# Kernel optimization log

Hardware: AMD Instinct MI355X
Metric: run time of the kernel (lower is better)

The kernel has to match this reference:

```python
import jax, jax.numpy as jnp
import numpy as np

EPS = 1e-8
HIDDEN = 200


def _dsmall(n, d):
    # torch: d = d*(d>eps) + eps*(d<=eps); n/d
    return n / jnp.where(d > EPS, d, EPS)


def _mp_match(v1, v2, w):
    # v1: (B,S,H); v2: (B,S,H) or (B,H); w: (L,H) -> (B,S,L)
    wt = w.T[None, None]                      # (1,1,H,L)
    a = v1[..., None] * wt                    # (B,S,H,L)
    if v2.ndim == 2:
        v2 = jnp.broadcast_to(v2[:, None, :], v1.shape)
    b = v2[..., None] * wt                    # (B,S,H,L)
    dot = jnp.sum(a * b, axis=2)
    na = jnp.linalg.norm(a, axis=2)
    nb = jnp.linalg.norm(b, axis=2)
    return dot / jnp.maximum(na * nb, EPS)    # cosine_similarity over H


def _mp_pairwise(v1, v2, w):
    # v1: (B,S1,H); v2: (B,S2,H); w: (L,H) -> (B,S1,S2,L)
    a = v1[:, None] * w[None, :, None]        # (B,L,S1,H)
    b = v2[:, None] * w[None, :, None]        # (B,L,S2,H)
    na = jnp.linalg.norm(a, axis=3, keepdims=True)   # (B,L,S1,1)
    nb = jnp.linalg.norm(b, axis=3, keepdims=True)   # (B,L,S2,1)
    n = jnp.einsum('blph,blqh->blpq', a, b)
    d = na * jnp.swapaxes(nb, 2, 3)
    return jnp.transpose(_dsmall(n, d), (0, 2, 3, 1))


def _attention(v1, v2):
    # cosine-similarity matrix (B,S1,S2)
    n1 = jnp.linalg.norm(v1, axis=2, keepdims=True)           # (B,S1,1)
    n2 = jnp.linalg.norm(v2, axis=2, keepdims=True)           # (B,S2,1)
    a = jnp.einsum('bph,bqh->bpq', v1, v2)
    return _dsmall(a, n1 * jnp.swapaxes(n2, 1, 2))


def _matching(con_p, con_h, w1, w2, w3, w4, w5, w6, w7, w8):
    p_fw, p_bw = con_p[..., :HIDDEN], con_p[..., HIDDEN:]
    h_fw, h_bw = con_h[..., :HIDDEN], con_h[..., HIDDEN:]

    # 1) full matching
    mv_p_full_fw = _mp_match(p_fw, h_fw[:, -1, :], w1)
    mv_p_full_bw = _mp_match(p_bw, h_bw[:, 0, :], w2)
    mv_h_full_fw = _mp_match(h_fw, p_fw[:, -1, :], w1)
    mv_h_full_bw = _mp_match(h_bw, p_bw[:, 0, :], w2)

    # 2) maxpooling matching
    mv_max_fw = _mp_pairwise(p_fw, h_fw, w3)  # (B,S1,S2,L)
    mv_max_bw = _mp_pairwise(p_bw, h_bw, w4)
    mv_p_max_fw = jnp.max(mv_max_fw, axis=2)
    mv_p_max_bw = jnp.max(mv_max_bw, axis=2)
    mv_h_max_fw = jnp.max(mv_max_fw, axis=1)
    mv_h_max_bw = jnp.max(mv_max_bw, axis=1)

    # 3) attentive matching (mean)
    att_fw = _attention(p_fw, h_fw)           # (B,S1,S2)
    att_bw = _attention(p_bw, h_bw)

    # sum of att_h over dim 2 is a matmul (same math, no (B,S1,S2,H) tensor)
    att_h_sum_fw = jnp.einsum('bpq,bqh->bph', att_fw, h_fw)
    att_h_sum_bw = jnp.einsum('bpq,bqh->bph', att_bw, h_bw)
    att_p_sum_fw = jnp.einsum('bpq,bph->bqh', att_fw, p_fw)
    att_p_sum_bw = jnp.einsum('bpq,bph->bqh', att_bw, p_bw)

    att_mean_h_fw = _dsmall(att_h_sum_fw, jnp.sum(att_fw, axis=2, keepdims=True))
    att_mean_h_bw = _dsmall(att_h_sum_bw, jnp.sum(att_bw, axis=2, keepdims=True))
    att_mean_p_fw = _dsmall(att_p_sum_fw, jnp.swapaxes(jnp.sum(att_fw, axis=1, keepdims=True), 1, 2))
    att_mean_p_bw = _dsmall(att_p_sum_bw, jnp.swapaxes(jnp.sum(att_bw, axis=1, keepdims=True), 1, 2))

    mv_p_att_mean_fw = _mp_match(p_fw, att_mean_h_fw, w5)
    mv_p_att_mean_bw = _mp_match(p_bw, att_mean_h_bw, w6)
    mv_h_att_mean_fw = _mp_match(h_fw, att_mean_p_fw, w5)
    mv_h_att_mean_bw = _mp_match(h_bw, att_mean_p_bw, w6)

    # 4) max-attentive matching (needs full (B,S1,S2,H) broadcast for the max)
    att_h_fw = h_fw[:, None, :, :] * att_fw[:, :, :, None]   # (B,S1,S2,H)
    att_h_bw = h_bw[:, None, :, :] * att_bw[:, :, :, None]
    att_p_fw = p_fw[:, :, None, :] * att_fw[:, :, :, None]
    att_p_bw = p_bw[:, :, None, :] * att_bw[:, :, :, None]

    att_max_h_fw = jnp.max(att_h_fw, axis=2)                 # (B,S1,H)
    att_max_h_bw = jnp.max(att_h_bw, axis=2)
    att_max_p_fw = jnp.max(att_p_fw, axis=1)                 # (B,S2,H)
    att_max_p_bw = jnp.max(att_p_bw, axis=1)

    mv_p_att_max_fw = _mp_match(p_fw, att_max_h_fw, w7)
    mv_p_att_max_bw = _mp_match(p_bw, att_max_h_bw, w8)
    mv_h_att_max_fw = _mp_match(h_fw, att_max_p_fw, w7)
    mv_h_att_max_bw = _mp_match(h_bw, att_max_p_bw, w8)

    mv_p = jnp.concatenate([mv_p_full_fw, mv_p_max_fw, mv_p_att_mean_fw, mv_p_att_max_fw,
                            mv_p_full_bw, mv_p_max_bw, mv_p_att_mean_bw, mv_p_att_max_bw], axis=2)
    mv_h = jnp.concatenate([mv_h_full_fw, mv_h_max_fw, mv_h_att_mean_fw, mv_h_att_max_fw,
                            mv_h_full_bw, mv_h_max_bw, mv_h_att_mean_bw, mv_h_att_max_bw], axis=2)
    # dropout is identity in inference mode
    return mv_p, mv_h


def setup_inputs() -> dict:
    key = jax.random.key(0)
    ks = jax.random.split(key, 10)
    B, S, H, L = 32, 64, HIDDEN, 20
    w_std = np.sqrt(2.0 / H)  # kaiming_normal fan_in
    inp = {
        'con_p': jax.random.normal(ks[0], (B, S, 2 * H), dtype=jnp.float32),
        'con_h': jax.random.normal(ks[1], (B, S, 2 * H), dtype=jnp.float32),
    }
    for i in range(8):
        inp[f'mp_w{i+1}'] = jax.random.normal(ks[2 + i], (L, H), dtype=jnp.float32) * w_std
    return inp


def reference(con_p, con_h, mp_w1, mp_w2, mp_w3, mp_w4, mp_w5, mp_w6, mp_w7, mp_w8):
    return _matching(con_p, con_h, mp_w1, mp_w2, mp_w3, mp_w4, mp_w5, mp_w6, mp_w7, mp_w8)
```

## Files before the change

### kernel.cpp

```cpp
#include <hip/hip_runtime.h>
#include <hip/hip_bf16.h>
#include <math.h>

#define EPS 1e-8f
#define BB 32
#define SS 64
#define HH 200
#define LL 20
#define KST 232
#define SST 68
#define MHS 200

typedef short bf16x8 __attribute__((ext_vector_type(8)));
typedef float f32x4 __attribute__((ext_vector_type(4)));

__device__ inline float bf2f(short u) {
    union { unsigned int i; float f; } v;
    v.i = ((unsigned int)(unsigned short)u) << 16;
    return v.f;
}

__global__ __launch_bounds__(512) void fused_all_kernel(
        const float* __restrict__ conp, const float* __restrict__ conh,
        const float* __restrict__ w1, const float* __restrict__ w2,
        const float* __restrict__ w3, const float* __restrict__ w4,
        const float* __restrict__ w5, const float* __restrict__ w6,
        const float* __restrict__ w7, const float* __restrict__ w8,
        float* __restrict__ out) {
    __shared__ __align__(16) float smem[19392];
    int t = threadIdx.x;

    int wg = ((blockIdx.x & 7) * 224) + (blockIdx.x >> 3);
    int grp = wg / 7;
    int rem = wg % 7;

    if (rem < 2) {
        __hip_bfloat16* AT = (__hip_bfloat16*)smem;
        __hip_bfloat16* BT = (__hip_bfloat16*)(smem + 1856);
        float* S_L  = smem + 9280;
        float* nrmA = smem + 10368;
        float* nrmB = smem + 10384;
        __hip_bfloat16* PB = (__hip_bfloat16*)smem;
        __hip_bfloat16* WB = (__hip_bfloat16*)(smem + 9280);
        float* meanL = smem + 12992;
        float* maxL  = smem + 16192;

        int blk = grp * 2 + rem;
        int qh = blk & 3;
        int sdb = blk >> 2;
        int b = sdb & 31, sd = sdb >> 5;
        int dir = sd & 1, side = sd >> 1;
        const float* selfb = side ? conh : conp;
        const float* oppb  = side ? conp : conh;
        int fidx = dir ? 0 : (SS - 1);
        const float* fvr = oppb + (b * SS + fidx) * (2 * HH) + dir * HH;

        int arow = t / 25, ack = t % 25;

        float xr[8], yv0[8];
        if (t < 400) {
            const float* xp = selfb + (b * SS + qh * 16 + arow) * (2 * HH) + dir * HH + ack * 8;
            *(float4*)&xr[0] = *(const float4*)xp; *(float4*)&xr[4] = *(const float4*)(xp + 4);
            *(float4*)&yv0[0] = *(const float4*)(fvr + ack * 8);
            *(float4*)&yv0[4] = *(const float4*)(fvr + ack * 8 + 4);
            __align__(16) __hip_bfloat16 r8[8];
#pragma unroll
            for (int i = 0; i < 8; ++i) r8[i] = __float2bfloat16(xr[i]);
            *(bf16x8*)&AT[arow * KST + ack * 8] = *(bf16x8*)r8;
        }
        {
            __align__(16) __hip_bfloat16 z8[8];
#pragma unroll
            for (int i = 0; i < 8; ++i) z8[i] = __float2bfloat16(0.f);
            if (t < 240) {
                if (t < 48) { int row = t / 3, ckp = 25 + t % 3;
                    *(bf16x8*)&AT[row * KST + ckp * 8] = *(bf16x8*)z8;
                } else { int e2 = t - 48; int row = e2 / 3, ckp = 25 + e2 % 3;
                    *(bf16x8*)&BT[row * KST + ckp * 8] = *(bf16x8*)z8;
                }
            }
        }
        for (int e = t; e < 1600; e += 512) {
            int rw = e / 25, ck = e % 25, k = ck * 8;
            const float* xp = oppb + (b * SS + rw) * (2 * HH) + dir * HH + k;
            float xv[8];
            *(float4*)&xv[0] = *(const float4*)xp; *(float4*)&xv[4] = *(const float4*)(xp + 4);
            __align__(16) __hip_bfloat16 r8[8];
#pragma unroll
            for (int i = 0; i < 8; ++i) r8[i] = __float2bfloat16(xv[i]);
            *(bf16x8*)&BT[rw * KST + k] = *(bf16x8*)r8;
        }
        __syncthreads();

        int wv_ = __builtin_amdgcn_readfirstlane(t >> 6);
        int lane = t & 63;
        int q = lane >> 4, c = lane & 15;

        if (wv_ < 4) {
            int ct = wv_;
            f32x4 acc = (f32x4){0.f, 0.f, 0.f, 0.f};
            for (int ks = 0; ks < 7; ++ks) {
                int kb = ks * 32 + q * 8;
                bf16x8 af  = *(const bf16x8*)&AT[c * KST + kb];
                bf16x8 bf_ = *(const bf16x8*)&BT[(ct * 16 + c) * KST + kb];
                acc = __builtin_amdgcn_mfma_f32_16x16x32_bf16(af, bf_, acc, 0, 0, 0);
            }
            int col = ct * 16 + c;
#pragma unroll
            for (int r = 0; r < 4; ++r) S_L[(q * 4 + r) * SST + col] = acc[r];
        } else {
            int dt = wv_ - 4;
            f32x4 accB = (f32x4){0.f, 0.f, 0.f, 0.f};
            for (int ks = 0; ks < 7; ++ks) {
                int kb = ks * 32 + q * 8;
                bf16x8 bf_ = *(const bf16x8*)&BT[(dt * 16 + c) * KST + kb];
                accB = __builtin_amdgcn_mfma_f32_16x16x32_bf16(bf_, bf_, accB, 0, 0, 0);
            }
            if ((c >> 2) == q) nrmB[dt * 16 + c] = accB[c & 3];
            if (dt == 0) {
                f32x4 accA = (f32x4){0.f, 0.f, 0.f, 0.f};
                for (int ks = 0; ks < 7; ++ks) {
                    int kb = ks * 32 + q * 8;
                    bf16x8 af = *(const bf16x8*)&AT[c * KST + kb];
                    accA = __builtin_amdgcn_mfma_f32_16x16x32_bf16(af, af, accA, 0, 0, 0);
                }
                if ((c >> 2) == q) nrmA[c] = accA[c & 3];
            }
        }
        __syncthreads();

        for (int e = t; e < 1024; e += 512) {
            int r_ = e >> 6, cc = e & 63;
            float ns = sqrtf(nrmA[r_]), no = sqrtf(nrmB[cc]);
            S_L[r_ * SST + cc] = S_L[r_ * SST + cc] / fmaxf(ns * no, EPS);
        }
        __syncthreads();

        float wf0[8], wf1[8], wf2[8];
        if (t < 500) {
            int wl = t / 25, wck = t % 25;
            const float* wp0 = (dir ? w2 : w1) + wl * HH + wck * 8;
            const float* wp1 = (dir ? w6 : w5) + wl * HH + wck * 8;
            const float* wp2 = (dir ? w8 : w7) + wl * HH + wck * 8;
            *(float4*)&wf0[0] = *(const float4*)wp0; *(float4*)&wf0[4] = *(const float4*)(wp0 + 4);
            *(float4*)&wf1[0] = *(const float4*)wp1; *(float4*)&wf1[4] = *(const float4*)(wp1 + 4);
            *(float4*)&wf2[0] = *(const float4*)wp2; *(float4*)&wf2[4] = *(const float4*)(wp2 + 4);
        }

        if (t < 400) {
            int s = arow, h0 = ack * 8;
            float sm = 0.f;
            float ms[8], mx[8];
#pragma unroll
            for (int i = 0; i < 8; ++i) { ms[i] = 0.f; mx[i] = -INFINITY; }
            for (int k = 0; k < 64; ++k) {
                float a = S_L[s * SST + k];
                sm += a;
                bf16x8 ov = *(const bf16x8*)&BT[k * KST + h0];
#pragma unroll
                for (int i = 0; i < 8; ++i) {
                    float tt = a * bf2f(ov[i]);
                    ms[i] += tt;
                    mx[i] = fmaxf(mx[i], tt);
                }
            }
            float dsv = fmaxf(sm, EPS);
#pragma unroll
            for (int i = 0; i < 8; ++i) ms[i] /= dsv;
            *(float4*)&meanL[s * MHS + h0]     = *(float4*)&ms[0];
            *(float4*)&meanL[s * MHS + h0 + 4] = *(float4*)&ms[4];
            *(float4*)&maxL[s * MHS + h0]      = *(float4*)&mx[0];
            *(float4*)&maxL[s * MHS + h0 + 4]  = *(float4*)&mx[4];
        }
        __syncthreads();

#pragma unroll
        for (int m = 0; m < 3; ++m) {
            if (t < 400) {
                float yv[8];
                if (m == 0) {
#pragma unroll
                    for (int i = 0; i < 8; ++i) yv[i] = yv0[i];
                } else {
                    const float* yL = (m == 1 ? meanL : maxL) + arow * MHS + ack * 8;
                    *(float4*)&yv[0] = *(const float4*)yL;
                    *(float4*)&yv[4] = *(const float4*)(yL + 4);
                }
                __align__(16) __hip_bfloat16 r1[8], r2[8];
#pragma unroll
                for (int i = 0; i < 8; ++i) {
                    r1[i] = __float2bfloat16(xr[i] * yv[i]);
                    r2[i] = __float2bfloat16(yv[i] * yv[i]);
                }
                if (m == 0) {
                    __align__(16) __hip_bfloat16 r0[8];
#pragma unroll
                    for (int i = 0; i < 8; ++i) r0[i] = __float2bfloat16(xr[i] * xr[i]);
                    *(bf16x8*)&PB[(0 * 16 + arow) * KST + ack * 8] = *(bf16x8*)r0;
                }
                *(bf16x8*)&PB[(1 * 16 + arow) * KST + ack * 8] = *(bf16x8*)r1;
                *(bf16x8*)&PB[(2 * 16 + arow) * KST + ack * 8] = *(bf16x8*)r2;
            }
            if (t < 500) {
                int wl = t / 25, wck = t % 25;
                __align__(16) __hip_bfloat16 wr[8];
                if (m == 0) {
#pragma unroll
                    for (int i = 0; i < 8; ++i) wr[i] = __float2bfloat16(wf0[i] * wf0[i]);
                } else if (m == 1) {
#pragma unroll
                    for (int i = 0; i < 8; ++i) wr[i] = __float2bfloat16(wf1[i] * wf1[i]);
                } else {
#pragma unroll
                    for (int i = 0; i < 8; ++i) wr[i] = __float2bfloat16(wf2[i] * wf2[i]);
                }
                *(bf16x8*)&WB[wl * KST + wck * 8] = *(bf16x8*)wr;
            }
            if (m == 0) {
                __align__(16) __hip_bfloat16 z8[8];
#pragma unroll
                for (int i = 0; i < 8; ++i) z8[i] = __float2bfloat16(0.f);
                for (int e = t; e < 540; e += 512) {
                    if (e < 144) { int row = e / 3, ckp = 25 + e % 3;
                        *(bf16x8*)&PB[row * KST + ckp * 8] = *(bf16x8*)z8;
                    } else if (e < 480) { int e2 = e - 144; int row = 20 + e2 / 28, ckp = e2 % 28;
                        *(bf16x8*)&WB[row * KST + ckp * 8] = *(bf16x8*)z8;
                    } else { int e2 = e - 480; int row = e2 / 3, ckp = 25 + e2 % 3;
                        *(bf16x8*)&WB[row * KST + ckp * 8] = *(bf16x8*)z8;
                    }
                }
            }
            __syncthreads();

            if (wv_ < 2) {
                int ntile = wv_;
                f32x4 accA = (f32x4){0.f, 0.f, 0.f, 0.f};
                f32x4 accD = (f32x4){0.f, 0.f, 0.f, 0.f};
                f32x4 accB = (f32x4){0.f, 0.f, 0.f, 0.f};
                for (int ks = 0; ks < 7; ++ks) {
                    int kb = ks * 32 + q * 8;
                    bf16x8 bfw = *(const bf16x8*)&WB[(ntile * 16 + c) * KST + kb];
                    bf16x8 a0 = *(const bf16x8*)&PB[(0 * 16 + c) * KST + kb];
                    bf16x8 a1 = *(const bf16x8*)&PB[(1 * 16 + c) * KST + kb];
                    bf16x8 a2 = *(const bf16x8*)&PB[(2 * 16 + c) * KST + kb];
                    accA = __builtin_amdgcn_mfma_f32_16x16x32_bf16(a0, bfw, accA, 0, 0, 0);
                    accD = __builtin_amdgcn_mfma_f32_16x16x32_bf16(a1, bfw, accD, 0, 0, 0);
                    accB = __builtin_amdgcn_mfma_f32_16x16x32_bf16(a2, bfw, accB, 0, 0, 0);
                }
                int l_ = ntile * 16 + c;
                if (l_ < LL) {
                    int chunk = (m == 0) ? 0 : (m == 1) ? 40 : 60;
#pragma unroll
                    for (int r = 0; r < 4; ++r) {
                        int s = qh * 16 + q * 4 + r;
                        float cosv = accD[r] / fmaxf(sqrtf(accA[r] * accB[r]), EPS);
                        out[side * (BB * SS * 160) + (b * SS + s) * 160 + dir * 80 + chunk + l_] = cosv;
                    }
                }
            }
            if (m < 2) __syncthreads();
        }
    } else {
        __hip_bfloat16* AT = (__hip_bfloat16*)smem;
        __hip_bfloat16* BT = (__hip_bfloat16*)(smem + 7424);
        float* cmL = smem + 14848;
        float* nA  = smem + 15104;
        float* nB  = smem + 15168;
        int blk = grp * 5 + (rem - 2);
        int l = blk % LL; int db = blk / LL; int b = db & 31; int dir = db >> 5;

        const float* wrow = (dir ? w4 : w3) + l * HH;
        const float* Ag = conp + dir * HH;
        const float* Bg = conh + dir * HH;

        for (int e = t; e < 64 * 28; e += 512) {
            int m = e / 28, ck = e - m * 28;
            int k = ck * 8;
            __align__(16) __hip_bfloat16 at8[8];
            __align__(16) __hip_bfloat16 bt8[8];
            if (k < HH) {
                const float* ap = Ag + (b * SS + m) * (2 * HH) + k;
                const float* bp = Bg + (b * SS + m) * (2 * HH) + k;
                const float* wp = wrow + k;
                float av[8], bv[8], wvv[8];
                *(float4*)&av[0]  = *(const float4*)ap; *(float4*)&av[4]  = *(const float4*)(ap + 4);
                *(float4*)&bv[0]  = *(const float4*)bp; *(float4*)&bv[4]  = *(const float4*)(bp + 4);
                *(float4*)&wvv[0] = *(const float4*)wp; *(float4*)&wvv[4] = *(const float4*)(wp + 4);
#pragma unroll
                for (int i = 0; i < 8; ++i) {
                    at8[i] = __float2bfloat16(av[i] * wvv[i]);
                    bt8[i] = __float2bfloat16(bv[i] * wvv[i]);
                }
            } else {
#pragma unroll
                for (int ii = 0; ii < 8; ++ii) { at8[ii] = __float2bfloat16(0.f); bt8[ii] = __float2bfloat16(0.f); }
            }
            *(bf16x8*)&AT[m * KST + k] = *(bf16x8*)at8;
            *(bf16x8*)&BT[m * KST + k] = *(bf16x8*)bt8;
        }
        __syncthreads();

        int wv_ = __builtin_amdgcn_readfirstlane(t >> 6);
        int lane = t & 63;
        int q = lane >> 4, c = lane & 15;
        int m0 = wv_ * 16;

        f32x4 acc[4];
#pragma unroll
        for (int ct = 0; ct < 4; ++ct) acc[ct] = (f32x4){0.f, 0.f, 0.f, 0.f};

        if (wv_ < 4) {
            for (int ks = 0; ks < 7; ++ks) {
                int kb = ks * 32 + q * 8;
                bf16x8 af = *(const bf16x8*)&AT[(m0 + c) * KST + kb];
#pragma unroll
                for (int ct = 0; ct < 4; ++ct) {
                    bf16x8 bf_ = *(const bf16x8*)&BT[(ct * 16 + c) * KST + kb];
                    acc[ct] = __builtin_amdgcn_mfma_f32_16x16x32_bf16(af, bf_, acc[ct], 0, 0, 0);
                }
            }
        } else {
            int d0 = (wv_ - 4) * 16;
            f32x4 accA = (f32x4){0.f, 0.f, 0.f, 0.f};
            f32x4 accB = (f32x4){0.f, 0.f, 0.f, 0.f};
            for (int ks = 0; ks < 7; ++ks) {
                int kb = ks * 32 + q * 8;
                bf16x8 af = *(const bf16x8*)&AT[(d0 + c) * KST + kb];
                bf16x8 bf_ = *(const bf16x8*)&BT[(d0 + c) * KST + kb];
                accA = __builtin_amdgcn_mfma_f32_16x16x32_bf16(af, af, accA, 0, 0, 0);
                accB = __builtin_amdgcn_mfma_f32_16x16x32_bf16(bf_, bf_, accB, 0, 0, 0);
            }
            if ((c >> 2) == q) { nA[d0 + c] = accA[c & 3]; nB[d0 + c] = accB[c & 3]; }
        }
        __syncthreads();

        if (wv_ < 4) {
            float na[4], nb[4];
#pragma unroll
            for (int r = 0; r < 4; ++r) na[r] = sqrtf(nA[m0 + q * 4 + r]);
#pragma unroll
            for (int ct = 0; ct < 4; ++ct) nb[ct] = sqrtf(nB[ct * 16 + c]);

            float rowm[4] = {-INFINITY, -INFINITY, -INFINITY, -INFINITY};
            float colm[4] = {-INFINITY, -INFINITY, -INFINITY, -INFINITY};
#pragma unroll
            for (int ct = 0; ct < 4; ++ct) {
#pragma unroll
                for (int r = 0; r < 4; ++r) {
                    float cv = acc[ct][r] / fmaxf(na[r] * nb[ct], EPS);
                    rowm[r] = fmaxf(rowm[r], cv);
                    colm[ct] = fmaxf(colm[ct], cv);
                }
            }

#pragma unroll
            for (int r = 0; r < 4; ++r) {
                float v = rowm[r];
                v = fmaxf(v, __shfl_xor(v, 1, 64));
                v = fmaxf(v, __shfl_xor(v, 2, 64));
                v = fmaxf(v, __shfl_xor(v, 4, 64));
                v = fmaxf(v, __shfl_xor(v, 8, 64));
                rowm[r] = v;
            }
            if (c == 0) {
#pragma unroll
                for (int r = 0; r < 4; ++r) {
                    int i = m0 + q * 4 + r;
                    out[(b * SS + i) * 160 + dir * 80 + 20 + l] = rowm[r];
                }
            }

#pragma unroll
            for (int ct = 0; ct < 4; ++ct) {
                float v = colm[ct];
                v = fmaxf(v, __shfl_xor(v, 16, 64));
                v = fmaxf(v, __shfl_xor(v, 32, 64));
                colm[ct] = v;
            }
            if (q == 0) {
#pragma unroll
                for (int ct = 0; ct < 4; ++ct) cmL[wv_ * 64 + ct * 16 + c] = colm[ct];
            }
        }
        __syncthreads();
        if (t < 64) {
            float m = fmaxf(fmaxf(cmL[t], cmL[64 + t]), fmaxf(cmL[128 + t], cmL[192 + t]));
            out[BB * SS * 160 + (b * SS + t) * 160 + dir * 80 + 20 + l] = m;
        }
    }
}

extern "C" void kernel_launch(void* const* d_in, const int* in_sizes, int n_in,
                              void* d_out, int out_size, void* d_ws, size_t ws_size,
                              hipStream_t stream) {
    const float* conp = (const float*)d_in[0];
    const float* conh = (const float*)d_in[1];
    const float* w1 = (const float*)d_in[2];
    const float* w2 = (const float*)d_in[3];
    const float* w3 = (const float*)d_in[4];
    const float* w4 = (const float*)d_in[5];
    const float* w5 = (const float*)d_in[6];
    const float* w6 = (const float*)d_in[7];
    const float* w7 = (const float*)d_in[8];
    const float* w8 = (const float*)d_in[9];
    float* out = (float*)d_out;
    (void)d_ws; (void)ws_size;

    fused_all_kernel<<<1792, 512, 0, stream>>>(conp, conh,
                                               w1, w2, w3, w4, w5, w6, w7, w8, out);
}
```

Baseline: 116.4 us.

## Compute attentive mean via f16 MFMA and max via packed f16 math

Switches the staged operands from bf16 to f16 and keeps the similarity tile in registers, writing a normalised f16 copy. It adds a transposed copy of the opposing sequence so one wave computes the attentive-mean vectors as an MFMA. The per-row divide by the attention sum becomes a constant scale, relying on the later cosine similarity being invariant to scaling y. The remaining waves compute the attentive max with packed f16x2 multiply and max. This removes the scalar fp32 64×200 mean/max loop and its LDS traffic, at the cost of f16 range and precision risk and an extra transpose step.

```diff
diff --git a/kernel.cpp b/kernel.cpp
--- a/kernel.cpp
+++ b/kernel.cpp
@@ -8,17 +8,14 @@
 #define HH 200
 #define LL 20
 #define KST 232
-#define SST 68
-#define MHS 200
+#define S16ST 72
+#define BHST 72
+#define MLST 208
 
 typedef short bf16x8 __attribute__((ext_vector_type(8)));
 typedef float f32x4 __attribute__((ext_vector_type(4)));
-
-__device__ inline float bf2f(short u) {
-    union { unsigned int i; float f; } v;
-    v.i = ((unsigned int)(unsigned short)u) << 16;
-    return v.f;
-}
+typedef _Float16 f16x8v __attribute__((ext_vector_type(8)));
+typedef _Float16 f16x2 __attribute__((ext_vector_type(2)));
 
 __global__ __launch_bounds__(512) void fused_all_kernel(
         const float* __restrict__ conp, const float* __restrict__ conh,
@@ -27,7 +24,7 @@
         const float* __restrict__ w5, const float* __restrict__ w6,
         const float* __restrict__ w7, const float* __restrict__ w8,
         float* __restrict__ out) {
-    __shared__ __align__(16) float smem[19392];
+    __shared__ __align__(16) float smem[19104];
     int t = threadIdx.x;
 
     int wg = ((blockIdx.x & 7) * 224) + (blockIdx.x >> 3);
@@ -35,15 +32,15 @@
     int rem = wg % 7;
 
     if (rem < 2) {
-        __hip_bfloat16* AT = (__hip_bfloat16*)smem;
-        __hip_bfloat16* BT = (__hip_bfloat16*)(smem + 1856);
-        float* S_L  = smem + 9280;
-        float* nrmA = smem + 10368;
-        float* nrmB = smem + 10384;
-        __hip_bfloat16* PB = (__hip_bfloat16*)smem;
-        __hip_bfloat16* WB = (__hip_bfloat16*)(smem + 9280);
-        float* meanL = smem + 12992;
-        float* maxL  = smem + 16192;
+        _Float16* AT16 = (_Float16*)smem;
+        _Float16* BT16 = (_Float16*)(smem + 1856);
+        _Float16* BHh  = (_Float16*)(smem + 9280);
+        _Float16* S16h = (_Float16*)(smem + 16768);
+        float* nrmA  = smem + 17344;
+        float* nrmB  = smem + 17360;
+        _Float16* meanLh = (_Float16*)(smem + 17440);
+        _Float16* PB = (_Float16*)smem;
+        _Float16* WB = (_Float16*)(smem + 5568);
 
         int blk = grp * 2 + rem;
         int qh = blk & 3;
@@ -63,20 +60,20 @@
             *(float4*)&xr[0] = *(const float4*)xp; *(float4*)&xr[4] = *(const float4*)(xp + 4);
             *(float4*)&yv0[0] = *(const float4*)(fvr + ack * 8);
             *(float4*)&yv0[4] = *(const float4*)(fvr + ack * 8 + 4);
-            __align__(16) __hip_bfloat16 r8[8];
-#pragma unroll
-            for (int i = 0; i < 8; ++i) r8[i] = __float2bfloat16(xr[i]);
-            *(bf16x8*)&AT[arow * KST + ack * 8] = *(bf16x8*)r8;
+            f16x8v r8;
+#pragma unroll
+            for (int i = 0; i < 8; ++i) r8[i] = (_Float16)xr[i];
+            *(f16x8v*)&AT16[arow * KST + ack * 8] = r8;
         }
         {
-            __align__(16) __hip_bfloat16 z8[8];
-#pragma unroll
-            for (int i = 0; i < 8; ++i) z8[i] = __float2bfloat16(0.f);
-            if (t < 240) {
+            f16x8v z8 = (f16x8v)(_Float16)0.f;
+            if (t < 312) {
                 if (t < 48) { int row = t / 3, ckp = 25 + t % 3;
-                    *(bf16x8*)&AT[row * KST + ckp * 8] = *(bf16x8*)z8;
-                } else { int e2 = t - 48; int row = e2 / 3, ckp = 25 + e2 % 3;
-                    *(bf16x8*)&BT[row * KST + ckp * 8] = *(bf16x8*)z8;
+                    *(f16x8v*)&AT16[row * KST + ckp * 8] = z8;
+                } else if (t < 240) { int e2 = t - 48; int row = e2 / 3, ckp = 25 + e2 % 3;
+                    *(f16x8v*)&BT16[row * KST + ckp * 8] = z8;
+                } else { int e2 = t - 240; int row = 200 + e2 / 9, c8 = (e2 % 9) * 8;
+                    *(f16x8v*)&BHh[row * BHST + c8] = z8;
                 }
             }
         }
@@ -85,10 +82,10 @@
             const float* xp = oppb + (b * SS + rw) * (2 * HH) + dir * HH + k;
             float xv[8];
             *(float4*)&xv[0] = *(const float4*)xp; *(float4*)&xv[4] = *(const float4*)(xp + 4);
-            __align__(16) __hip_bfloat16 r8[8];
-#pragma unroll
-            for (int i = 0; i < 8; ++i) r8[i] = __float2bfloat16(xv[i]);
-            *(bf16x8*)&BT[rw * KST + k] = *(bf16x8*)r8;
+            f16x8v r8;
+#pragma unroll
+            for (int i = 0; i < 8; ++i) r8[i] = (_Float16)xv[i];
+            *(f16x8v*)&BT16[rw * KST + k] = r8;
         }
         __syncthreads();
 
@@ -96,43 +93,51 @@
         int lane = t & 63;
         int q = lane >> 4, c = lane & 15;
 
+        f32x4 accS = (f32x4){0.f, 0.f, 0.f, 0.f};
         if (wv_ < 4) {
             int ct = wv_;
-            f32x4 acc = (f32x4){0.f, 0.f, 0.f, 0.f};
             for (int ks = 0; ks < 7; ++ks) {
                 int kb = ks * 32 + q * 8;
-                bf16x8 af  = *(const bf16x8*)&AT[c * KST + kb];
-                bf16x8 bf_ = *(const bf16x8*)&BT[(ct * 16 + c) * KST + kb];
-                acc = __builtin_amdgcn_mfma_f32_16x16x32_bf16(af, bf_, acc, 0, 0, 0);
-            }
-            int col = ct * 16 + c;
-#pragma unroll
-            for (int r = 0; r < 4; ++r) S_L[(q * 4 + r) * SST + col] = acc[r];
+                f16x8v af  = *(const f16x8v*)&AT16[c * KST + kb];
+                f16x8v bf_ = *(const f16x8v*)&BT16[(ct * 16 + c) * KST + kb];
+                accS = __builtin_amdgcn_mfma_f32_16x16x32_f16(af, bf_, accS, 0, 0, 0);
+            }
         } else {
             int dt = wv_ - 4;
             f32x4 accB = (f32x4){0.f, 0.f, 0.f, 0.f};
             for (int ks = 0; ks < 7; ++ks) {
                 int kb = ks * 32 + q * 8;
-                bf16x8 bf_ = *(const bf16x8*)&BT[(dt * 16 + c) * KST + kb];
-                accB = __builtin_amdgcn_mfma_f32_16x16x32_bf16(bf_, bf_, accB, 0, 0, 0);
+                f16x8v bf_ = *(const f16x8v*)&BT16[(dt * 16 + c) * KST + kb];
+                accB = __builtin_amdgcn_mfma_f32_16x16x32_f16(bf_, bf_, accB, 0, 0, 0);
             }
             if ((c >> 2) == q) nrmB[dt * 16 + c] = accB[c & 3];
             if (dt == 0) {
                 f32x4 accA = (f32x4){0.f, 0.f, 0.f, 0.f};
                 for (int ks = 0; ks < 7; ++ks) {
                     int kb = ks * 32 + q * 8;
-                    bf16x8 af = *(const bf16x8*)&AT[c * KST + kb];
-                    accA = __builtin_amdgcn_mfma_f32_16x16x32_bf16(af, af, accA, 0, 0, 0);
+                    f16x8v af = *(const f16x8v*)&AT16[c * KST + kb];
+                    accA = __builtin_amdgcn_mfma_f32_16x16x32_f16(af, af, accA, 0, 0, 0);
                 }
                 if ((c >> 2) == q) nrmA[c] = accA[c & 3];
-            }
-        }
-        __syncthreads();
-
-        for (int e = t; e < 1024; e += 512) {
-            int r_ = e >> 6, cc = e & 63;
-            float ns = sqrtf(nrmA[r_]), no = sqrtf(nrmB[cc]);
-            S_L[r_ * SST + cc] = S_L[r_ * SST + cc] / fmaxf(ns * no, EPS);
+            } else {
+                for (int ch = dt - 1; ch < 25; ch += 3) {
+                    f16x8v v = *(const f16x8v*)&BT16[lane * KST + ch * 8];
+#pragma unroll
+                    for (int i = 0; i < 8; ++i) BHh[(ch * 8 + i) * BHST + lane] = v[i];
+                }
+            }
+        }
+        __syncthreads();
+
+        if (wv_ < 4) {
+            int col = wv_ * 16 + c;
+            float no = sqrtf(nrmB[col]);
+#pragma unroll
+            for (int r = 0; r < 4; ++r) {
+                int row = q * 4 + r;
+                float ns = sqrtf(nrmA[row]);
+                S16h[row * S16ST + col] = (_Float16)(accS[r] / fmaxf(ns * no, EPS));
+            }
         }
         __syncthreads();
 
@@ -147,30 +152,48 @@
             *(float4*)&wf2[0] = *(const float4*)wp2; *(float4*)&wf2[4] = *(const float4*)(wp2 + 4);
         }
 
-        if (t < 400) {
-            int s = arow, h0 = ack * 8;
-            float sm = 0.f;
-            float ms[8], mx[8];
-#pragma unroll
-            for (int i = 0; i < 8; ++i) { ms[i] = 0.f; mx[i] = -INFINITY; }
-            for (int k = 0; k < 64; ++k) {
-                float a = S_L[s * SST + k];
-                sm += a;
-                bf16x8 ov = *(const bf16x8*)&BT[k * KST + h0];
-#pragma unroll
-                for (int i = 0; i < 8; ++i) {
-                    float tt = a * bf2f(ov[i]);
-                    ms[i] += tt;
-                    mx[i] = fmaxf(mx[i], tt);
-                }
-            }
-            float dsv = fmaxf(sm, EPS);
-#pragma unroll
-            for (int i = 0; i < 8; ++i) ms[i] /= dsv;
-            *(float4*)&meanL[s * MHS + h0]     = *(float4*)&ms[0];
-            *(float4*)&meanL[s * MHS + h0 + 4] = *(float4*)&ms[4];
-            *(float4*)&maxL[s * MHS + h0]      = *(float4*)&mx[0];
-            *(float4*)&maxL[s * MHS + h0 + 4]  = *(float4*)&mx[4];
+        f16x2 mx0, mx1, mx2, mx3;
+        {
+            f16x2 ninf = {(_Float16)(-INFINITY), (_Float16)(-INFINITY)};
+            mx0 = ninf; mx1 = ninf; mx2 = ninf; mx3 = ninf;
+        }
+        if (wv_ == 7) {
+            for (int nt = 0; nt < 13; ++nt) {
+                f32x4 macc = (f32x4){0.f, 0.f, 0.f, 0.f};
+#pragma unroll
+                for (int k2 = 0; k2 < 2; ++k2) {
+                    int kb = k2 * 32 + q * 8;
+                    f16x8v sa = *(const f16x8v*)&S16h[c * S16ST + kb];
+                    f16x8v bh = *(const f16x8v*)&BHh[(nt * 16 + c) * BHST + kb];
+                    macc = __builtin_amdgcn_mfma_f32_16x16x32_f16(sa, bh, macc, 0, 0, 0);
+                }
+                int h = nt * 16 + c;
+                if (h < 200) {
+#pragma unroll
+                    for (int r = 0; r < 4; ++r)
+                        meanLh[(q * 4 + r) * MLST + h] = (_Float16)(macc[r] * 0.125f);
+                }
+            }
+        } else if (t < 400) {
+            const _Float16* srow = &S16h[arow * S16ST];
+            const _Float16* bcol = &BT16[ack * 8];
+            for (int kg = 0; kg < 8; ++kg) {
+                f16x8v sr = *(const f16x8v*)&srow[kg * 8];
+#pragma unroll
+                for (int kk = 0; kk < 8; ++kk) {
+                    _Float16 sh = sr[kk];
+                    f16x2 sv = {sh, sh};
+                    f16x8v bv = *(const f16x8v*)&bcol[(kg * 8 + kk) * KST];
+                    f16x2 p0 = sv * __builtin_shufflevector(bv, bv, 0, 1);
+                    f16x2 p1 = sv * __builtin_shufflevector(bv, bv, 2, 3);
+                    f16x2 p2 = sv * __builtin_shufflevector(bv, bv, 4, 5);
+                    f16x2 p3 = sv * __builtin_shufflevector(bv, bv, 6, 7);
+                    mx0 = __builtin_elementwise_max(mx0, p0);
+                    mx1 = __builtin_elementwise_max(mx1, p1);
+                    mx2 = __builtin_elementwise_max(mx2, p2);
+                    mx3 = __builtin_elementwise_max(mx3, p3);
+                }
+            }
         }
         __syncthreads();
 
@@ -181,52 +204,55 @@
                 if (m == 0) {
 #pragma unroll
                     for (int i = 0; i < 8; ++i) yv[i] = yv0[i];
+                } else if (m == 1) {
+                    f16x8v yl = *(const f16x8v*)&meanLh[arow * MLST + ack * 8];
+#pragma unroll
+                    for (int i = 0; i < 8; ++i) yv[i] = (float)yl[i];
                 } else {
-                    const float* yL = (m == 1 ? meanL : maxL) + arow * MHS + ack * 8;
-                    *(float4*)&yv[0] = *(const float4*)yL;
-                    *(float4*)&yv[4] = *(const float4*)(yL + 4);
-                }
-                __align__(16) __hip_bfloat16 r1[8], r2[8];
+                    yv[0] = (float)mx0[0]; yv[1] = (float)mx0[1];
+                    yv[2] = (float)mx1[0]; yv[3] = (float)mx1[1];
+                    yv[4] = (float)mx2[0]; yv[5] = (float)mx2[1];
+                    yv[6] = (float)mx3[0]; yv[7] = (float)mx3[1];
+                }
+                f16x8v r1, r2;
 #pragma unroll
                 for (int i = 0; i < 8; ++i) {
-                    r1[i] = __float2bfloat16(xr[i] * yv[i]);
-                    r2[i] = __float2bfloat16(yv[i] * yv[i]);
+                    r1[i] = (_Float16)(xr[i] * yv[i]);
+                    r2[i] = (_Float16)(yv[i] * yv[i]);
                 }
                 if (m == 0) {
-                    __align__(16) __hip_bfloat16 r0[8];
-#pragma unroll
-                    for (int i = 0; i < 8; ++i) r0[i] = __float2bfloat16(xr[i] * xr[i]);
-                    *(bf16x8*)&PB[(0 * 16 + arow) * KST + ack * 8] = *(bf16x8*)r0;
-                }
-                *(bf16x8*)&PB[(1 * 16 + arow) * KST + ack * 8] = *(bf16x8*)r1;
-                *(bf16x8*)&PB[(2 * 16 + arow) * KST + ack * 8] = *(bf16x8*)r2;
+                    f16x8v r0;
+#pragma unroll
+                    for (int i = 0; i < 8; ++i) r0[i] = (_Float16)(xr[i] * xr[i]);
+                    *(f16x8v*)&PB[(0 * 16 + arow) * KST + ack * 8] = r0;
+                }
+                *(f16x8v*)&PB[(1 * 16 + arow) * KST + ack * 8] = r1;
+                *(f16x8v*)&PB[(2 * 16 + arow) * KST + ack * 8] = r2;
             }
             if (t < 500) {
                 int wl = t / 25, wck = t % 25;
-                __align__(16) __hip_bfloat16 wr[8];
+                f16x8v wr;
                 if (m == 0) {
 #pragma unroll
-                    for (int i = 0; i < 8; ++i) wr[i] = __float2bfloat16(wf0[i] * wf0[i]);
+                    for (int i = 0; i < 8; ++i) wr[i] = (_Float16)(wf0[i] * wf0[i]);
                 } else if (m == 1) {
 #pragma unroll
-                    for (int i = 0; i < 8; ++i) wr[i] = __float2bfloat16(wf1[i] * wf1[i]);
+                    for (int i = 0; i < 8; ++i) wr[i] = (_Float16)(wf1[i] * wf1[i]);
                 } else {
 #pragma unroll
-                    for (int i = 0; i < 8; ++i) wr[i] = __float2bfloat16(wf2[i] * wf2[i]);
-                }
-                *(bf16x8*)&WB[wl * KST + wck * 8] = *(bf16x8*)wr;
+                    for (int i = 0; i < 8; ++i) wr[i] = (_Float16)(wf2[i] * wf2[i]);
+                }
+                *(f16x8v*)&WB[wl * KST + wck * 8] = wr;
             }
             if (m == 0) {
-                __align__(16) __hip_bfloat16 z8[8];
-#pragma unroll
-                for (int i = 0; i < 8; ++i) z8[i] = __float2bfloat16(0.f);
+                f16x8v z8 = (f16x8v)(_Float16)0.f;
                 for (int e = t; e < 540; e += 512) {
                     if (e < 144) { int row = e / 3, ckp = 25 + e % 3;
-                        *(bf16x8*)&PB[row * KST + ckp * 8] = *(bf16x8*)z8;
+                        *(f16x8v*)&PB[row * KST + ckp * 8] = z8;
                     } else if (e < 480) { int e2 = e - 144; int row = 20 + e2 / 28, ckp = e2 % 28;
-                        *(bf16x8*)&WB[row * KST + ckp * 8] = *(bf16x8*)z8;
+                        *(f16x8v*)&WB[row * KST + ckp * 8] = z8;
                     } else { int e2 = e - 480; int row = e2 / 3, ckp = 25 + e2 % 3;
-                        *(bf16x8*)&WB[row * KST + ckp * 8] = *(bf16x8*)z8;
+                        *(f16x8v*)&WB[row * KST + ckp * 8] = z8;
                     }
                 }
             }
@@ -239,13 +265,13 @@
                 f32x4 accB = (f32x4){0.f, 0.f, 0.f, 0.f};
                 for (int ks = 0; ks < 7; ++ks) {
                     int kb = ks * 32 + q * 8;
-                    bf16x8 bfw = *(const bf16x8*)&WB[(ntile * 16 + c) * KST + kb];
-                    bf16x8 a0 = *(const bf16x8*)&PB[(0 * 16 + c) * KST + kb];
-                    bf16x8 a1 = *(const bf16x8*)&PB[(1 * 16 + c) * KST + kb];
-                    bf16x8 a2 = *(const bf16x8*)&PB[(2 * 16 + c) * KST + kb];
-                    accA = __builtin_amdgcn_mfma_f32_16x16x32_bf16(a0, bfw, accA, 0, 0, 0);
-                    accD = __builtin_amdgcn_mfma_f32_16x16x32_bf16(a1, bfw, accD, 0, 0, 0);
-                    accB = __builtin_amdgcn_mfma_f32_16x16x32_bf16(a2, bfw, accB, 0, 0, 0);
+                    f16x8v bfw = *(const f16x8v*)&WB[(ntile * 16 + c) * KST + kb];
+                    f16x8v a0 = *(const f16x8v*)&PB[(0 * 16 + c) * KST + kb];
+                    f16x8v a1 = *(const f16x8v*)&PB[(1 * 16 + c) * KST + kb];
+                    f16x8v a2 = *(const f16x8v*)&PB[(2 * 16 + c) * KST + kb];
+                    accA = __builtin_amdgcn_mfma_f32_16x16x32_f16(a0, bfw, accA, 0, 0, 0);
+                    accD = __builtin_amdgcn_mfma_f32_16x16x32_f16(a1, bfw, accD, 0, 0, 0);
+                    accB = __builtin_amdgcn_mfma_f32_16x16x32_f16(a2, bfw, accB, 0, 0, 0);
                 }
                 int l_ = ntile * 16 + c;
                 if (l_ < LL) {
```

Result: faster. 107.4 us (-7.8%).
